# Performance work log

Measured on AMD Instinct MI355X. Metric: run time of the kernel, lower is better.

The kernel has to match this reference:

```python
import jax, jax.numpy as jnp
import numpy as np

B, C, N = 8, 128, 4096  # (batch, channels=dim, time); F = N//2+1 = 2049 (odd)


def setup_inputs() -> dict:
    key = jax.random.key(0)
    ks = jax.random.split(key, 7)
    s = 1.0 / np.sqrt(C)
    return {
        "x_in": jax.random.normal(ks[0], (B, C, N), dtype=jnp.float32),
        "W_K": jax.random.normal(ks[1], (C, C), dtype=jnp.float32) * s,
        "b_K": jax.random.normal(ks[2], (C,), dtype=jnp.float32) * s,
        "W_V": jax.random.normal(ks[3], (C, C), dtype=jnp.float32) * s,
        "b_V": jax.random.normal(ks[4], (C,), dtype=jnp.float32) * s,
        "w_high": jax.random.normal(ks[5], (C, 2), dtype=jnp.float32) * 0.02,
        "threshold_param": jax.random.uniform(ks[6], (1,), dtype=jnp.float32) * 0.5,
    }


def reference(x_in, W_K, b_K, W_V, b_V, w_high, threshold_param):
    x = jnp.transpose(x_in, (0, 2, 1)).astype(jnp.float32)  # (B, N, C)
    _, n, c = x.shape
    x_fft = jnp.fft.rfft(x, axis=1, norm="ortho")            # (B, F, C) complex64
    K = jnp.fft.rfft(x @ W_K.T + b_K, axis=1, norm="ortho")  # (B, F, C)
    V = jnp.fft.rfft(x @ W_V.T + b_V, axis=1, norm="ortho")  # (B, F, C)
    scale = c ** (-0.5)
    # complex attention scores (no conjugation, matching torch.matmul(Q, K^T))
    attn = jnp.einsum("bfc,bgc->bfg", x_fft, K) * scale      # (B, F, F) complex
    attn = jax.nn.softmax(jnp.abs(attn), axis=-1)            # real softmax of |scores|
    context = jnp.einsum("bfg,bgc->bfc", attn.astype(x_fft.dtype), V)
    # adaptive high-frequency mask
    energy = jnp.sum(jnp.abs(x_fft) ** 2, axis=-1)           # (B, F)
    median_energy = jnp.median(energy, axis=1, keepdims=True)
    normalized = energy / (median_energy + 1e-6)
    threshold = jnp.quantile(normalized, threshold_param[0])  # global quantile
    mask = (normalized > threshold)[:, :, None]               # (B, F, 1)
    w_hi = w_high[:, 0] + 1j * w_high[:, 1]                   # (C,) complex
    context = context + jnp.where(mask, x_fft, 0.0) * w_hi
    out = jnp.fft.irfft(context, n=n, axis=1, norm="ortho")  # (B, N, C) float32
    return jnp.transpose(out, (0, 2, 1))                      # (B, C, N)
```

## Files before the change

kernel.cpp:

```cpp
#include <hip/hip_runtime.h>
#include <math.h>

#define NB 8
#define NC 128
#define NT 4096
#define NF 2049
#define FP 2176
#define LDP 72

typedef __bf16 bf16;
typedef __bf16 bf16x2 __attribute__((ext_vector_type(2)));
typedef __bf16 bf16x8 __attribute__((ext_vector_type(8)));
typedef float f32x4 __attribute__((ext_vector_type(4)));
typedef unsigned int uint32x4 __attribute__((ext_vector_type(4)));

__device__ __forceinline__ void async16(const bf16* g, bf16* l) {
    __builtin_amdgcn_global_load_lds(
        (const __attribute__((address_space(1))) void*)g,
        (__attribute__((address_space(3))) void*)l, 16, 0, 0);
}

__device__ __forceinline__ bf16x8 derive_b2(bf16x8 v) {
    uint32x4 u = __builtin_bit_cast(uint32x4, v);
#pragma unroll
    for (int i = 0; i < 4; ++i)
        u[i] = (((u[i] >> 16) | (u[i] << 16)) ^ 0x00008000u);
    return __builtin_bit_cast(bf16x8, u);
}

__device__ __forceinline__ void fft4096(float2* buf) {
    for (int half = 1; half < NT; half <<= 1) {
        __syncthreads();
        const float fac = -(float)M_PI / (float)half;
        for (int t = threadIdx.x; t < NT / 2; t += 256) {
            int pos = t & (half - 1);
            int i = 2 * t - pos;
            int j = i + half;
            float sw, cw;
            __sincosf(fac * (float)pos, &sw, &cw);
            float2 u = buf[i], v = buf[j];
            float vr = v.x * cw - v.y * sw;
            float vi = v.x * sw + v.y * cw;
            buf[i] = make_float2(u.x + vr, u.y + vi);
            buf[j] = make_float2(u.x - vr, u.y - vi);
        }
    }
    __syncthreads();
}

__global__ __launch_bounds__(256) void fft_fwd_kernel(const float* __restrict__ x_in,
                                                      float2* __restrict__ Xc) {
    __shared__ float2 buf[NT];
    int bc = blockIdx.x;
    const float* xrow = x_in + (size_t)bc * NT;
    for (int i = threadIdx.x; i < NT; i += 256) {
        int r = __brev((unsigned)i) >> 20;
        buf[r] = make_float2(xrow[i], 0.0f);
    }
    fft4096(buf);
    const float inv = 1.0f / 64.0f;
    float2* orow = Xc + (size_t)bc * NF;
    for (int f = threadIdx.x; f < NF; f += 256) {
        float2 v = buf[f];
        orow[f] = make_float2(v.x * inv, v.y * inv);
    }
}

__global__ __launch_bounds__(256) void xt_kernel(const float2* __restrict__ Xc,
                                                 float2* __restrict__ Xf2,
                                                 bf16* __restrict__ Xb) {
    __shared__ float2 tile[64][65];
    int blk = blockIdx.x;
    int b = blk / 68;
    int t2 = blk % 68;
    int c0 = (t2 / 34) * 64;
    int f0 = (t2 % 34) * 64;
    int t = threadIdx.x;
    int fl = t & 63, cc = t >> 6;
#pragma unroll
    for (int cb = 0; cb < 16; ++cb) {
        int cl = cb * 4 + cc;
        int f = f0 + fl;
        float2 v = make_float2(0.f, 0.f);
        if (f < NF) v = Xc[((size_t)b * NC + c0 + cl) * NF + f];
        tile[fl][cl] = v;
    }
    __syncthreads();
    int chl = t & 63, ww = t >> 6;
#pragma unroll
    for (int wb = 0; wb < 16; ++wb) {
        int fl2 = wb * 4 + ww;
        int f = f0 + fl2;
        float2 v = tile[fl2][chl];
        if (f < NF) Xf2[((size_t)b * NF + f) * 128 + c0 + chl] = v;
        bf16x2 p;
        p[0] = (bf16)v.x; p[1] = (bf16)v.y;
        *(bf16x2*)&Xb[((size_t)b * FP + f) * 256 + 2 * (c0 + chl)] = p;
    }
}

__global__ __launch_bounds__(256) void wpack_kernel(const float* __restrict__ W_K,
                                                    const float* __restrict__ W_V,
                                                    bf16* __restrict__ Wk1,
                                                    bf16* __restrict__ Av) {
    int idx = blockIdx.x * 256 + threadIdx.x;
    if (idx < 256 * 256) {
        int n = idx >> 8, k = idx & 255;
        int c = k >> 1;
        int j = n >> 1;
        float v = 0.f;
        if (!(n & 1) && !(k & 1)) v = W_K[j * NC + c];
        else if ((n & 1) && (k & 1)) v = -W_K[j * NC + c];
        Wk1[idx] = (bf16)v;
        float v2 = 0.f;
        if (!(n & 1) && !(k & 1)) v2 = W_V[j * NC + c];
        else if ((n & 1) && (k & 1)) v2 = W_V[j * NC + c];
        Av[idx] = (bf16)v2;
    }
}

__global__ __launch_bounds__(256, 2) void kvgemm_kernel(const bf16* __restrict__ Xb,
                                                        const bf16* __restrict__ Wk1,
                                                        bf16* __restrict__ K1) {
    __shared__ bf16 As[128][LDP];
    __shared__ bf16 Bs[128][LDP];
    int blk = blockIdx.x;
    int b = blk & 7;
    int t2 = blk >> 3;
    int g0 = (t2 >> 1) * 128;
    int n0 = (t2 & 1) * 128;
    int tid = threadIdx.x;
    int wave = tid >> 6, lane = tid & 63;
    int m = lane & 15, quad = lane >> 4;
    int row_off = (wave & 1) * 64, col_off = (wave >> 1) * 64;

    f32x4 acc[4][4] = {};
    const bf16* Abase = Xb + ((size_t)b * FP + g0) * 256;
    const bf16* Bbase = Wk1 + (size_t)n0 * 256;
    int r0 = tid >> 3, c0 = (tid & 7) * 8;

    for (int kk = 0; kk < 256; kk += 64) {
        __syncthreads();
#pragma unroll
        for (int s = 0; s < 4; ++s) {
            int r = r0 + 32 * s;
            *(bf16x8*)&As[r][c0] = *(const bf16x8*)&Abase[(size_t)r * 256 + kk + c0];
            *(bf16x8*)&Bs[r][c0] = *(const bf16x8*)&Bbase[(size_t)r * 256 + kk + c0];
        }
        __syncthreads();
#pragma unroll
        for (int k2 = 0; k2 < 64; k2 += 32) {
            bf16x8 a[4], bb[4];
            int kq = k2 + quad * 8;
#pragma unroll
            for (int i = 0; i < 4; ++i) a[i] = *(const bf16x8*)&As[row_off + i * 16 + m][kq];
#pragma unroll
            for (int j = 0; j < 4; ++j) bb[j] = *(const bf16x8*)&Bs[col_off + j * 16 + m][kq];
#pragma unroll
            for (int i = 0; i < 4; ++i)
#pragma unroll
                for (int j = 0; j < 4; ++j)
                    acc[i][j] = __builtin_amdgcn_mfma_f32_16x16x32_bf16(a[i], bb[j], acc[i][j], 0, 0, 0);
        }
    }
#pragma unroll
    for (int i = 0; i < 4; ++i)
#pragma unroll
        for (int j = 0; j < 4; ++j)
#pragma unroll
            for (int r = 0; r < 4; ++r) {
                int row = g0 + row_off + i * 16 + quad * 4 + r;
                int col = n0 + col_off + j * 16 + m;
                K1[((size_t)b * FP + row) * 256 + col] = (bf16)acc[i][j][r];
            }
}

__global__ __launch_bounds__(256, 2) void vtgemm_kernel(const bf16* __restrict__ Av,
                                                        const bf16* __restrict__ Xb,
                                                        bf16* __restrict__ Vt) {
    __shared__ bf16 As[128][LDP];
    __shared__ bf16 Bs[128][LDP];
    int blk = blockIdx.x;
    int b = blk & 7;
    int t2 = blk >> 3;
    int g0 = (t2 >> 1) * 128;
    int n0 = (t2 & 1) * 128;
    int tid = threadIdx.x;
    int wave = tid >> 6, lane = tid & 63;
    int m = lane & 15, quad = lane >> 4;
    int row_off = (wave & 1) * 64, col_off = (wave >> 1) * 64;

    f32x4 acc[4][4] = {};
    const bf16* Abase = Av + (size_t)n0 * 256;
    const bf16* Bbase = Xb + ((size_t)b * FP + g0) * 256;
    int r0 = tid >> 3, c0 = (tid & 7) * 8;

    for (int kk = 0; kk < 256; kk += 64) {
        __syncthreads();
#pragma unroll
        for (int s = 0; s < 4; ++s) {
            int r = r0 + 32 * s;
            *(bf16x8*)&As[r][c0] = *(const bf16x8*)&Abase[(size_t)r * 256 + kk + c0];
            *(bf16x8*)&Bs[r][c0] = *(const bf16x8*)&Bbase[(size_t)r * 256 + kk + c0];
        }
        __syncthreads();
#pragma unroll
        for (int k2 = 0; k2 < 64; k2 += 32) {
            bf16x8 a[4], bb[4];
            int kq = k2 + quad * 8;
#pragma unroll
            for (int i = 0; i < 4; ++i) a[i] = *(const bf16x8*)&As[row_off + i * 16 + m][kq];
#pragma unroll
            for (int j = 0; j < 4; ++j) bb[j] = *(const bf16x8*)&Bs[col_off + j * 16 + m][kq];
#pragma unroll
            for (int i = 0; i < 4; ++i)
#pragma unroll
                for (int j = 0; j < 4; ++j)
                    acc[i][j] = __builtin_amdgcn_mfma_f32_16x16x32_bf16(a[i], bb[j], acc[i][j], 0, 0, 0);
        }
    }
#pragma unroll
    for (int i = 0; i < 4; ++i)
#pragma unroll
        for (int j = 0; j < 4; ++j)
#pragma unroll
            for (int r = 0; r < 4; ++r) {
                int row = n0 + row_off + i * 16 + quad * 4 + r;
                int col = g0 + col_off + j * 16 + m;
                Vt[((size_t)b * 256 + row) * FP + col] = (bf16)acc[i][j][r];
            }
}

__global__ __launch_bounds__(128) void biasfix_kernel(const float* __restrict__ b_K,
                                                      const float* __restrict__ b_V,
                                                      bf16* __restrict__ K1,
                                                      bf16* __restrict__ Vt) {
    int b = blockIdx.x;
    int j = threadIdx.x;
    float bk = 64.0f * b_K[j], bv = 64.0f * b_V[j];
    size_t o = (size_t)b * FP * 256;
    K1[o + 2 * j] = (bf16)((float)K1[o + 2 * j] + bk);
    size_t ov = ((size_t)b * 256 + 2 * j) * FP;
    Vt[ov] = (bf16)((float)Vt[ov] + bv);
}

__global__ __launch_bounds__(256) void energy_kernel(const float* __restrict__ Xf,
                                                     float* __restrict__ energy) {
    int idx = blockIdx.x * 256 + threadIdx.x;
    if (idx >= NB * NF) return;
    const float4* row = (const float4*)(Xf + (size_t)idx * 2 * NC);
    float e = 0.f;
    for (int i = 0; i < 64; ++i) {
        float4 v = row[i];
        e += v.x * v.x + v.y * v.y + v.z * v.z + v.w * v.w;
    }
    energy[idx] = e;
}

__global__ __launch_bounds__(256) void median_kernel(const float* __restrict__ energy,
                                                     float* __restrict__ med) {
    int blk = blockIdx.x;
    int b = blk / 9, chunk = blk % 9;
    __shared__ __align__(16) float e[2052];
    for (int i = threadIdx.x; i < 2052; i += 256)
        e[i] = (i < NF) ? energy[b * NF + i] : INFINITY;
    __syncthreads();
    int i = chunk * 256 + threadIdx.x;
    float ei = (i < NF) ? e[i] : 0.f;
    int rank = 0;
#pragma unroll 4
    for (int j4 = 0; j4 < 513; ++j4) {
        float4 v = ((const float4*)e)[j4];
        int j = j4 * 4;
        rank += (v.x < ei) || (v.x == ei && j + 0 < i);
        rank += (v.y < ei) || (v.y == ei && j + 1 < i);
        rank += (v.z < ei) || (v.z == ei && j + 2 < i);
        rank += (v.w < ei) || (v.w == ei && j + 3 < i);
    }
    if (i < NF && rank == 1024) med[b] = ei;
}

__global__ __launch_bounds__(256) void norm_kernel(const float* __restrict__ energy,
                                                   const float* __restrict__ med,
                                                   float* __restrict__ nrm) {
    int idx = blockIdx.x * 256 + threadIdx.x;
    if (idx >= NB * NF) return;
    int b = idx / NF;
    nrm[idx] = energy[idx] / (med[b] + 1e-6f);
}

__global__ __launch_bounds__(256) void rankpart_kernel(const float* __restrict__ nrm,
                                                       int* __restrict__ rankpart) {
    const int n = NB * NF;
    int cb = blockIdx.x / 17;
    int chunk = blockIdx.x % 17;
    __shared__ __align__(16) float cdata[1024];
    int base = chunk * 1024;
    for (int t = threadIdx.x; t < 1024; t += 256)
        cdata[t] = (base + t < n) ? nrm[base + t] : INFINITY;
    __syncthreads();
    int i = cb * 256 + threadIdx.x;
    if (i >= n) return;
    float ei = nrm[i];
    int rank = 0;
#pragma unroll 8
    for (int t4 = 0; t4 < 256; ++t4) {
        float4 v = ((const float4*)cdata)[t4];
        int j = base + t4 * 4;
        rank += (v.x < ei) || (v.x == ei && j + 0 < i);
        rank += (v.y < ei) || (v.y == ei && j + 1 < i);
        rank += (v.z < ei) || (v.z == ei && j + 2 < i);
        rank += (v.w < ei) || (v.w == ei && j + 3 < i);
    }
    rankpart[(size_t)i * 17 + chunk] = rank;
}

__global__ __launch_bounds__(256) void rankreduce_kernel(const int* __restrict__ rankpart,
                                                         const float* __restrict__ nrm,
                                                         const float* __restrict__ q,
                                                         float* __restrict__ vk) {
    const int n = NB * NF;
    int i = blockIdx.x * 256 + threadIdx.x;
    if (i >= n) return;
    int rank = 0;
    const int* rp = rankpart + (size_t)i * 17;
#pragma unroll
    for (int c = 0; c < 17; ++c) rank += rp[c];
    double pos = (double)q[0] * (double)(n - 1);
    int k0 = (int)floor(pos);
    int k1 = min(k0 + 1, n - 1);
    if (rank == k0) vk[0] = nrm[i];
    if (rank == k1) vk[1] = nrm[i];
}

__global__ void thresh_kernel(const float* __restrict__ vk,
                              const float* __restrict__ q,
                              float* __restrict__ thr) {
    if (threadIdx.x == 0 && blockIdx.x == 0) {
        const int n = NB * NF;
        double pos = (double)q[0] * (double)(n - 1);
        double k0 = floor(pos);
        double frac = pos - k0;
        thr[0] = (float)((double)vk[0] + ((double)vk[1] - (double)vk[0]) * frac);
    }
}

__global__ __launch_bounds__(256, 2) void score_kernel(const bf16* __restrict__ Xb,
                                                       const bf16* __restrict__ K1,
                                                       bf16* __restrict__ S) {
    __shared__ __align__(16) char smem[34816];
    bf16* As  = (bf16*)smem;
    bf16* B1s = (bf16*)(smem + 16384);
    int blk = blockIdx.x;
    int b = blk & 7;
    int t2 = blk >> 3;
    int f0 = (t2 / 17) * 128;
    int g0 = (t2 % 17) * 128;
    int tid = threadIdx.x;
    int wave = tid >> 6, lane = tid & 63;
    int m = lane & 15, quad = lane >> 4;
    int row_off = (wave & 1) * 64, col_off = (wave >> 1) * 64;

    f32x4 accRe[4][4] = {};
    f32x4 accIm[4][4] = {};
    const bf16* Abase = Xb + ((size_t)b * FP + f0) * 256;
    const bf16* Kbase = K1 + ((size_t)b * FP + g0) * 256;
    int lrow = lane >> 3;
    int cswz = (lane & 7) ^ lrow;
    int mk = m & 7;

    for (int kk = 0; kk < 256; kk += 64) {
        __syncthreads();
#pragma unroll
        for (int t = 0; t < 4; ++t) {
            int r0 = wave * 32 + t * 8;
            async16(Abase + (size_t)(r0 + lrow) * 256 + kk + cswz * 8, As + r0 * 64);
            async16(Kbase + (size_t)(r0 + lrow) * 256 + kk + cswz * 8, B1s + r0 * 64);
        }
        __syncthreads();
#pragma unroll
        for (int k2 = 0; k2 < 64; k2 += 32) {
            bf16x8 a[4], b1[4], b2[4];
            int cb = k2 >> 3;
            int pos = ((cb + quad) ^ mk) << 3;
#pragma unroll
            for (int i = 0; i < 4; ++i)
                a[i] = *(const bf16x8*)&As[(row_off + i * 16 + m) * 64 + pos];
#pragma unroll
            for (int j = 0; j < 4; ++j) {
                b1[j] = *(const bf16x8*)&B1s[(col_off + j * 16 + m) * 64 + pos];
                b2[j] = derive_b2(b1[j]);
            }
#pragma unroll
            for (int i = 0; i < 4; ++i)
#pragma unroll
                for (int j = 0; j < 4; ++j) {
                    accRe[i][j] = __builtin_amdgcn_mfma_f32_16x16x32_bf16(a[i], b1[j], accRe[i][j], 0, 0, 0);
                    accIm[i][j] = __builtin_amdgcn_mfma_f32_16x16x32_bf16(a[i], b2[j], accIm[i][j], 0, 0, 0);
                }
        }
    }
    const float SCALE = 0.08838834764831845f;
    __syncthreads();
    bf16 (*Cs)[136] = (bf16(*)[136])smem;
#pragma unroll
    for (int i = 0; i < 4; ++i)
#pragma unroll
        for (int j = 0; j < 4; ++j)
#pragma unroll
            for (int r = 0; r < 4; ++r) {
                float re = accRe[i][j][r], im = accIm[i][j][r];
                Cs[row_off + i * 16 + quad * 4 + r][col_off + j * 16 + m] =
                    (bf16)(sqrtf(re * re + im * im) * SCALE);
            }
    __syncthreads();
    bf16* Sb = S + (size_t)b * FP * FP;
    int row = tid >> 1, half = tid & 1;
    const bf16* src = &Cs[row][half * 64];
    bf16* dst = Sb + (size_t)(f0 + row) * FP + g0 + half * 64;
#pragma unroll
    for (int u = 0; u < 8; ++u)
        *(bf16x8*)&dst[u * 8] = *(const bf16x8*)&src[u * 8];
}

__global__ __launch_bounds__(256) void softmax_kernel(bf16* __restrict__ S) {
    int bf = blockIdx.x;
    int b = bf / NF, f = bf % NF;
    bf16* row = S + ((size_t)b * FP + f) * FP;
    int t = threadIdx.x;
    __shared__ float red[256];
    bf16x8 raw = *(const bf16x8*)&row[t * 8];
    float tail = (t == 0) ? (float)row[2048] : -1e30f;
    float v[8];
    float mx = tail;
#pragma unroll
    for (int u = 0; u < 8; ++u) { v[u] = (float)raw[u]; mx = fmaxf(mx, v[u]); }
    red[t] = mx;
    __syncthreads();
    for (int s = 128; s > 0; s >>= 1) {
        if (t < s) red[t] = fmaxf(red[t], red[t + s]);
        __syncthreads();
    }
    float mval = red[0];
    __syncthreads();
    float sum = 0.f;
#pragma unroll
    for (int u = 0; u < 8; ++u) { v[u] = __expf(v[u] - mval); sum += v[u]; }
    float tex = 0.f;
    if (t == 0) { tex = __expf(tail - mval); sum += tex; }
    red[t] = sum;
    __syncthreads();
    for (int s = 128; s > 0; s >>= 1) {
        if (t < s) red[t] += red[t + s];
        __syncthreads();
    }
    float inv = 1.f / red[0];
    bf16x8 outv;
#pragma unroll
    for (int u = 0; u < 8; ++u) outv[u] = (bf16)(v[u] * inv);
    *(bf16x8*)&row[t * 8] = outv;
    if (t == 0) row[2048] = (bf16)(tex * inv);
    if (t < FP - NF) row[NF + t] = (bf16)0.f;
}

__global__ __launch_bounds__(256, 2) void context_kernel(const bf16* __restrict__ P,
                                                         const bf16* __restrict__ Vt,
                                                         float* __restrict__ Ctx) {
    __shared__ bf16 Ps[64][LDP];
    __shared__ bf16 Vs[256][LDP];
    int blk = blockIdx.x;
    int b = blk & 7;
    int f0 = (blk >> 3) * 64;
    int tid = threadIdx.x;
    int wave = tid >> 6, lane = tid & 63;
    int m = lane & 15, quad = lane >> 4;
    int col_off = wave * 64;

    f32x4 acc[4][4] = {};
    const bf16* Pbase = P + ((size_t)b * FP + f0) * FP;
    const bf16* Vbase = Vt + (size_t)b * 256 * FP;
    int r0 = tid >> 3, c0 = (tid & 7) * 8;

    for (int kk = 0; kk < FP; kk += 64) {
        __syncthreads();
#pragma unroll
        for (int s = 0; s < 2; ++s) {
            int r = r0 + 32 * s;
            *(bf16x8*)&Ps[r][c0] = *(const bf16x8*)&Pbase[(size_t)r * FP + kk + c0];
        }
#pragma unroll
        for (int s = 0; s < 8; ++s) {
            int r = r0 + 32 * s;
            *(bf16x8*)&Vs[r][c0] = *(const bf16x8*)&Vbase[(size_t)r * FP + kk + c0];
        }
        __syncthreads();
#pragma unroll
        for (int k2 = 0; k2 < 64; k2 += 32) {
            bf16x8 a[4], bb[4];
            int kq = k2 + quad * 8;
#pragma unroll
            for (int i = 0; i < 4; ++i) a[i] = *(const bf16x8*)&Ps[i * 16 + m][kq];
#pragma unroll
            for (int j = 0; j < 4; ++j) bb[j] = *(const bf16x8*)&Vs[col_off + j * 16 + m][kq];
#pragma unroll
            for (int i = 0; i < 4; ++i)
#pragma unroll
                for (int j = 0; j < 4; ++j)
                    acc[i][j] = __builtin_amdgcn_mfma_f32_16x16x32_bf16(a[i], bb[j], acc[i][j], 0, 0, 0);
        }
    }
#pragma unroll
    for (int i = 0; i < 4; ++i)
#pragma unroll
        for (int j = 0; j < 4; ++j)
#pragma unroll
            for (int r = 0; r < 4; ++r) {
                int row = f0 + i * 16 + quad * 4 + r;
                int col = col_off + j * 16 + m;
                if (row < NF) Ctx[((size_t)b * NF + row) * 256 + col] = acc[i][j][r];
            }
}

__global__ __launch_bounds__(256) void ctxt_kernel(const float2* __restrict__ Ctx2,
                                                   const float2* __restrict__ Xf2,
                                                   const float* __restrict__ nrm,
                                                   const float* __restrict__ thr,
                                                   const float* __restrict__ w_high,
                                                   float* __restrict__ Ctxt) {
    __shared__ float2 tile[64][33];
    int blk = blockIdx.x;
    int b = blk / 132;
    int t2 = blk % 132;
    int cp0 = (t2 / 33) * 32;
    int f0 = (t2 % 33) * 64;
    int t = threadIdx.x;
    float thrv = thr[0];
    int cpl = t & 31, rr = t >> 5;
#pragma unroll
    for (int rb = 0; rb < 8; ++rb) {
        int fl = rb * 8 + rr;
        int f = f0 + fl;
        float2 v = make_float2(0.f, 0.f);
        if (f < NF) {
            size_t idx = ((size_t)b * NF + f) * 128 + cp0 + cpl;
            v = Ctx2[idx];
            if (nrm[b * NF + f] > thrv) {
                float2 x = Xf2[idx];
                int c = cp0 + cpl;
                float wr = w_high[2 * c], wi = w_high[2 * c + 1];
                v.x += x.x * wr - x.y * wi;
                v.y += x.x * wi + x.y * wr;
            }
        }
        tile[fl][cpl] = v;
    }
    __syncthreads();
    int fl = t & 63, ww = t >> 6;
#pragma unroll
    for (int wb = 0; wb < 16; ++wb) {
        int chl = wb * 4 + ww;
        int f = f0 + fl;
        if (f < NF) {
            float2 v = tile[fl][chl >> 1];
            Ctxt[((size_t)b * 256 + 2 * cp0 + chl) * NF + f] = (chl & 1) ? v.y : v.x;
        }
    }
}

__global__ __launch_bounds__(256) void fft_inv_kernel(const float* __restrict__ Ctxt,
                                                      float* __restrict__ out) {
    __shared__ float2 buf[NT];
    int bc = blockIdx.x, b = bc >> 7, c = bc & 127;
    const float* base = Ctxt + ((size_t)b * 256 + 2 * c) * NF;
    const float* basei = base + NF;
    for (int f = threadIdx.x; f < NT; f += 256) {
        float re, im;
        if (f <= NT / 2) {
            re = base[f];
            im = -basei[f];
        } else {
            int g = NT - f;
            re = base[g];
            im = basei[g];
        }
        int r = __brev((unsigned)f) >> 20;
        buf[r] = make_float2(re, im);
    }
    fft4096(buf);
    float* orow = out + (size_t)bc * NT;
    const float inv = 1.0f / 64.0f;
    for (int n = threadIdx.x; n < NT; n += 256) orow[n] = buf[n].x * inv;
}

extern "C" void kernel_launch(void* const* d_in, const int* in_sizes, int n_in,
                              void* d_out, int out_size, void* d_ws, size_t ws_size,
                              hipStream_t stream) {
    const float* x_in = (const float*)d_in[0];
    const float* W_K = (const float*)d_in[1];
    const float* b_K = (const float*)d_in[2];
    const float* W_V = (const float*)d_in[3];
    const float* b_V = (const float*)d_in[4];
    const float* w_high = (const float*)d_in[5];
    const float* qpar = (const float*)d_in[6];
    float* out = (float*)d_out;

    char* w = (char*)d_ws;
    const size_t SPECB = (size_t)NB * NF * 256 * 4;
    float* Xf = (float*)w;            w += SPECB;
    float* Ctx = (float*)w;           w += SPECB;
    float* energy = (float*)w;        w += (size_t)NB * NF * 4;
    float* med = (float*)w;           w += 64;
    float* nrm = (float*)w;           w += (size_t)NB * NF * 4;
    float* vk = (float*)w;            w += 64;
    float* thr = (float*)w;           w += 64;
    w = (char*)(((uintptr_t)w + 255) & ~(uintptr_t)255);
    int* rankpart = (int*)w;          w += (size_t)16640 * 17 * 4;
    w = (char*)(((uintptr_t)w + 255) & ~(uintptr_t)255);
    bf16* S = (bf16*)w;               w += (size_t)NB * FP * FP * 2;
    bf16* Xb = (bf16*)w;              w += (size_t)NB * FP * 256 * 2;
    bf16* K1 = (bf16*)w;              w += (size_t)NB * FP * 256 * 2;
    bf16* Vt = (bf16*)w;              w += (size_t)NB * 256 * FP * 2;
    bf16* Wk1 = (bf16*)w;             w += (size_t)256 * 256 * 2;
    bf16* Av = (bf16*)w;              w += (size_t)256 * 256 * 2;
    float2* Xc = (float2*)S;
    float* Ctxt = (float*)Xb;

    fft_fwd_kernel<<<NB * NC, 256, 0, stream>>>(x_in, Xc);
    xt_kernel<<<NB * 2 * 34, 256, 0, stream>>>(Xc, (float2*)Xf, Xb);
    wpack_kernel<<<256, 256, 0, stream>>>(W_K, W_V, Wk1, Av);
    kvgemm_kernel<<<NB * 17 * 2, 256, 0, stream>>>(Xb, Wk1, K1);
    vtgemm_kernel<<<NB * 17 * 2, 256, 0, stream>>>(Av, Xb, Vt);
    biasfix_kernel<<<NB, 128, 0, stream>>>(b_K, b_V, K1, Vt);
    energy_kernel<<<(NB * NF + 255) / 256, 256, 0, stream>>>(Xf, energy);
    median_kernel<<<NB * 9, 256, 0, stream>>>(energy, med);
    norm_kernel<<<(NB * NF + 255) / 256, 256, 0, stream>>>(energy, med, nrm);
    rankpart_kernel<<<65 * 17, 256, 0, stream>>>(nrm, rankpart);
    rankreduce_kernel<<<65, 256, 0, stream>>>(rankpart, nrm, qpar, vk);
    thresh_kernel<<<1, 64, 0, stream>>>(vk, qpar, thr);
    score_kernel<<<NB * 17 * 17, 256, 0, stream>>>(Xb, K1, S);
    softmax_kernel<<<NB * NF, 256, 0, stream>>>(S);
    context_kernel<<<NB * 33, 256, 0, stream>>>(S, Vt, Ctx);
    ctxt_kernel<<<NB * 4 * 33, 256, 0, stream>>>((const float2*)Ctx, (const float2*)Xf,
                                                 nrm, thr, w_high, Ctxt);
    fft_inv_kernel<<<NB * NC, 256, 0, stream>>>(Ctxt, out);
}
```

Before: 433.8 us.

## Fuse score, softmax and context GEMMs into a single flash-attention kernel

Replaces the separate score GEMM, row softmax and context GEMM kernels with one kernel that uses an online softmax. Each block keeps 64 query rows resident and streams K and V tiles through shared memory, computing |score| tiles, running max/sum and PV accumulation in registers. This removes the large bf16 score matrix and its write/read/rewrite passes through global memory, and the score workspace is dropped, with the FFT scratch now aliased into Ctx. The trade-off is that all the score compute is serialised into only 264 blocks, with several barriers per tile and no double-buffering, so latency may be exposed.

```diff
diff --git a/kernel.cpp b/kernel.cpp
--- a/kernel.cpp
+++ b/kernel.cpp
@@ -345,180 +345,174 @@
     }
 }
 
-__global__ __launch_bounds__(256, 2) void score_kernel(const bf16* __restrict__ Xb,
+__global__ __launch_bounds__(256, 2) void flash_kernel(const bf16* __restrict__ Xb,
                                                        const bf16* __restrict__ K1,
-                                                       bf16* __restrict__ S) {
-    __shared__ __align__(16) char smem[34816];
-    bf16* As  = (bf16*)smem;
-    bf16* B1s = (bf16*)(smem + 16384);
-    int blk = blockIdx.x;
-    int b = blk & 7;
-    int t2 = blk >> 3;
-    int f0 = (t2 / 17) * 128;
-    int g0 = (t2 % 17) * 128;
-    int tid = threadIdx.x;
-    int wave = tid >> 6, lane = tid & 63;
-    int m = lane & 15, quad = lane >> 4;
-    int row_off = (wave & 1) * 64, col_off = (wave >> 1) * 64;
-
-    f32x4 accRe[4][4] = {};
-    f32x4 accIm[4][4] = {};
-    const bf16* Abase = Xb + ((size_t)b * FP + f0) * 256;
-    const bf16* Kbase = K1 + ((size_t)b * FP + g0) * 256;
-    int lrow = lane >> 3;
-    int cswz = (lane & 7) ^ lrow;
-    int mk = m & 7;
-
-    for (int kk = 0; kk < 256; kk += 64) {
-        __syncthreads();
-#pragma unroll
-        for (int t = 0; t < 4; ++t) {
-            int r0 = wave * 32 + t * 8;
-            async16(Abase + (size_t)(r0 + lrow) * 256 + kk + cswz * 8, As + r0 * 64);
-            async16(Kbase + (size_t)(r0 + lrow) * 256 + kk + cswz * 8, B1s + r0 * 64);
-        }
-        __syncthreads();
-#pragma unroll
-        for (int k2 = 0; k2 < 64; k2 += 32) {
-            bf16x8 a[4], b1[4], b2[4];
-            int cb = k2 >> 3;
-            int pos = ((cb + quad) ^ mk) << 3;
-#pragma unroll
-            for (int i = 0; i < 4; ++i)
-                a[i] = *(const bf16x8*)&As[(row_off + i * 16 + m) * 64 + pos];
-#pragma unroll
-            for (int j = 0; j < 4; ++j) {
-                b1[j] = *(const bf16x8*)&B1s[(col_off + j * 16 + m) * 64 + pos];
-                b2[j] = derive_b2(b1[j]);
-            }
-#pragma unroll
-            for (int i = 0; i < 4; ++i)
-#pragma unroll
-                for (int j = 0; j < 4; ++j) {
-                    accRe[i][j] = __builtin_amdgcn_mfma_f32_16x16x32_bf16(a[i], b1[j], accRe[i][j], 0, 0, 0);
-                    accIm[i][j] = __builtin_amdgcn_mfma_f32_16x16x32_bf16(a[i], b2[j], accIm[i][j], 0, 0, 0);
-                }
-        }
-    }
-    const float SCALE = 0.08838834764831845f;
-    __syncthreads();
-    bf16 (*Cs)[136] = (bf16(*)[136])smem;
-#pragma unroll
-    for (int i = 0; i < 4; ++i)
-#pragma unroll
-        for (int j = 0; j < 4; ++j)
-#pragma unroll
-            for (int r = 0; r < 4; ++r) {
-                float re = accRe[i][j][r], im = accIm[i][j][r];
-                Cs[row_off + i * 16 + quad * 4 + r][col_off + j * 16 + m] =
-                    (bf16)(sqrtf(re * re + im * im) * SCALE);
-            }
-    __syncthreads();
-    bf16* Sb = S + (size_t)b * FP * FP;
-    int row = tid >> 1, half = tid & 1;
-    const bf16* src = &Cs[row][half * 64];
-    bf16* dst = Sb + (size_t)(f0 + row) * FP + g0 + half * 64;
-#pragma unroll
-    for (int u = 0; u < 8; ++u)
-        *(bf16x8*)&dst[u * 8] = *(const bf16x8*)&src[u * 8];
-}
-
-__global__ __launch_bounds__(256) void softmax_kernel(bf16* __restrict__ S) {
-    int bf = blockIdx.x;
-    int b = bf / NF, f = bf % NF;
-    bf16* row = S + ((size_t)b * FP + f) * FP;
-    int t = threadIdx.x;
-    __shared__ float red[256];
-    bf16x8 raw = *(const bf16x8*)&row[t * 8];
-    float tail = (t == 0) ? (float)row[2048] : -1e30f;
-    float v[8];
-    float mx = tail;
-#pragma unroll
-    for (int u = 0; u < 8; ++u) { v[u] = (float)raw[u]; mx = fmaxf(mx, v[u]); }
-    red[t] = mx;
-    __syncthreads();
-    for (int s = 128; s > 0; s >>= 1) {
-        if (t < s) red[t] = fmaxf(red[t], red[t + s]);
-        __syncthreads();
-    }
-    float mval = red[0];
-    __syncthreads();
-    float sum = 0.f;
-#pragma unroll
-    for (int u = 0; u < 8; ++u) { v[u] = __expf(v[u] - mval); sum += v[u]; }
-    float tex = 0.f;
-    if (t == 0) { tex = __expf(tail - mval); sum += tex; }
-    red[t] = sum;
-    __syncthreads();
-    for (int s = 128; s > 0; s >>= 1) {
-        if (t < s) red[t] += red[t + s];
-        __syncthreads();
-    }
-    float inv = 1.f / red[0];
-    bf16x8 outv;
-#pragma unroll
-    for (int u = 0; u < 8; ++u) outv[u] = (bf16)(v[u] * inv);
-    *(bf16x8*)&row[t * 8] = outv;
-    if (t == 0) row[2048] = (bf16)(tex * inv);
-    if (t < FP - NF) row[NF + t] = (bf16)0.f;
-}
-
-__global__ __launch_bounds__(256, 2) void context_kernel(const bf16* __restrict__ P,
-                                                         const bf16* __restrict__ Vt,
-                                                         float* __restrict__ Ctx) {
-    __shared__ bf16 Ps[64][LDP];
-    __shared__ bf16 Vs[256][LDP];
+                                                       const bf16* __restrict__ Vt,
+                                                       float* __restrict__ Ctx) {
+    __shared__ __align__(16) char smem[65536];
+    bf16* As = (bf16*)smem;
+    bf16* KV = (bf16*)(smem + 32768);
+    bf16* Pw = (bf16*)(smem + 32768 + 16384);
     int blk = blockIdx.x;
     int b = blk & 7;
     int f0 = (blk >> 3) * 64;
     int tid = threadIdx.x;
     int wave = tid >> 6, lane = tid & 63;
     int m = lane & 15, quad = lane >> 4;
-    int col_off = wave * 64;
-
-    f32x4 acc[4][4] = {};
-    const bf16* Pbase = P + ((size_t)b * FP + f0) * FP;
-    const bf16* Vbase = Vt + (size_t)b * 256 * FP;
-    int r0 = tid >> 3, c0 = (tid & 7) * 8;
-
-    for (int kk = 0; kk < FP; kk += 64) {
-        __syncthreads();
-#pragma unroll
-        for (int s = 0; s < 2; ++s) {
-            int r = r0 + 32 * s;
-            *(bf16x8*)&Ps[r][c0] = *(const bf16x8*)&Pbase[(size_t)r * FP + kk + c0];
-        }
-#pragma unroll
-        for (int s = 0; s < 8; ++s) {
-            int r = r0 + 32 * s;
-            *(bf16x8*)&Vs[r][c0] = *(const bf16x8*)&Vbase[(size_t)r * FP + kk + c0];
-        }
-        __syncthreads();
-#pragma unroll
-        for (int k2 = 0; k2 < 64; k2 += 32) {
-            bf16x8 a[4], bb[4];
-            int kq = k2 + quad * 8;
-#pragma unroll
-            for (int i = 0; i < 4; ++i) a[i] = *(const bf16x8*)&Ps[i * 16 + m][kq];
-#pragma unroll
-            for (int j = 0; j < 4; ++j) bb[j] = *(const bf16x8*)&Vs[col_off + j * 16 + m][kq];
-#pragma unroll
-            for (int i = 0; i < 4; ++i)
-#pragma unroll
-                for (int j = 0; j < 4; ++j)
-                    acc[i][j] = __builtin_amdgcn_mfma_f32_16x16x32_bf16(a[i], bb[j], acc[i][j], 0, 0, 0);
-        }
-    }
-#pragma unroll
-    for (int i = 0; i < 4; ++i)
-#pragma unroll
-        for (int j = 0; j < 4; ++j)
+    int lrow = lane >> 3;
+    int cswz = (lane & 7) ^ lrow;
+    int mk = m & 7;
+    const float SCALE = 0.08838834764831845f;
+
+    const bf16* Ab = Xb + ((size_t)b * FP + f0) * 256;
+    const bf16* Kb = K1 + (size_t)b * FP * 256;
+    const bf16* Vb = Vt + (size_t)b * 256 * FP;
+
+#pragma unroll
+    for (int p = 0; p < 4; ++p)
+#pragma unroll
+        for (int t = 0; t < 2; ++t) {
+            int r0 = wave * 16 + t * 8;
+            async16(Ab + (size_t)(r0 + lrow) * 256 + p * 64 + cswz * 8,
+                    As + p * 4096 + r0 * 64);
+        }
+
+    float mrow[4] = {-1e30f, -1e30f, -1e30f, -1e30f};
+    float lsum[4] = {0.f, 0.f, 0.f, 0.f};
+    f32x4 o[16] = {};
+
+    for (int gi = 0; gi < 33; ++gi) {
+        int g0 = gi * 64;
+        __syncthreads();
+#pragma unroll
+        for (int p = 0; p < 4; ++p)
+#pragma unroll
+            for (int t = 0; t < 2; ++t) {
+                int r0 = wave * 16 + t * 8;
+                async16(Kb + (size_t)(g0 + r0 + lrow) * 256 + p * 64 + cswz * 8,
+                        KV + p * 4096 + r0 * 64);
+            }
+        __syncthreads();
+
+        f32x4 accRe[4] = {};
+        f32x4 accIm[4] = {};
+#pragma unroll
+        for (int ks = 0; ks < 8; ++ks) {
+            int p = ks >> 1;
+            int pos = (((ks & 1) * 4 + quad) ^ mk) << 3;
+            bf16x8 a = *(const bf16x8*)&As[p * 4096 + (wave * 16 + m) * 64 + pos];
+#pragma unroll
+            for (int j2 = 0; j2 < 4; ++j2) {
+                bf16x8 b1 = *(const bf16x8*)&KV[p * 4096 + (j2 * 16 + m) * 64 + pos];
+                bf16x8 b2 = derive_b2(b1);
+                accRe[j2] = __builtin_amdgcn_mfma_f32_16x16x32_bf16(a, b1, accRe[j2], 0, 0, 0);
+                accIm[j2] = __builtin_amdgcn_mfma_f32_16x16x32_bf16(a, b2, accIm[j2], 0, 0, 0);
+            }
+        }
+
+        float pv[4][4];
+        float tmax[4] = {-1e30f, -1e30f, -1e30f, -1e30f};
+#pragma unroll
+        for (int j2 = 0; j2 < 4; ++j2) {
+            int gcol = g0 + j2 * 16 + m;
+            bool valid = (gcol <= 2048);
 #pragma unroll
             for (int r = 0; r < 4; ++r) {
-                int row = f0 + i * 16 + quad * 4 + r;
-                int col = col_off + j * 16 + m;
-                if (row < NF) Ctx[((size_t)b * NF + row) * 256 + col] = acc[i][j][r];
-            }
+                float re = accRe[j2][r], im = accIm[j2][r];
+                float s = valid ? sqrtf(re * re + im * im) * SCALE : -1e30f;
+                pv[j2][r] = s;
+                tmax[r] = fmaxf(tmax[r], s);
+            }
+        }
+#pragma unroll
+        for (int r = 0; r < 4; ++r) {
+            tmax[r] = fmaxf(tmax[r], __shfl_xor(tmax[r], 1));
+            tmax[r] = fmaxf(tmax[r], __shfl_xor(tmax[r], 2));
+            tmax[r] = fmaxf(tmax[r], __shfl_xor(tmax[r], 4));
+            tmax[r] = fmaxf(tmax[r], __shfl_xor(tmax[r], 8));
+        }
+        float alpha[4], rs[4];
+#pragma unroll
+        for (int r = 0; r < 4; ++r) {
+            float mn = fmaxf(mrow[r], tmax[r]);
+            alpha[r] = __expf(mrow[r] - mn);
+            mrow[r] = mn;
+            rs[r] = 0.f;
+        }
+#pragma unroll
+        for (int j2 = 0; j2 < 4; ++j2)
+#pragma unroll
+            for (int r = 0; r < 4; ++r) {
+                float e = __expf(pv[j2][r] - mrow[r]);
+                pv[j2][r] = e;
+                rs[r] += e;
+            }
+#pragma unroll
+        for (int r = 0; r < 4; ++r) {
+            rs[r] += __shfl_xor(rs[r], 1);
+            rs[r] += __shfl_xor(rs[r], 2);
+            rs[r] += __shfl_xor(rs[r], 4);
+            rs[r] += __shfl_xor(rs[r], 8);
+            lsum[r] = lsum[r] * alpha[r] + rs[r];
+        }
+#pragma unroll
+        for (int j = 0; j < 16; ++j)
+#pragma unroll
+            for (int r = 0; r < 4; ++r) o[j][r] *= alpha[r];
+
+        __syncthreads();
+#pragma unroll
+        for (int t = 0; t < 4; ++t) {
+            int n0 = wave * 32 + t * 8;
+            async16(Vb + (size_t)(n0 + lrow) * FP + g0 + cswz * 8, KV + n0 * 64);
+        }
+#pragma unroll
+        for (int j2 = 0; j2 < 4; ++j2)
+#pragma unroll
+            for (int r = 0; r < 4; ++r)
+                Pw[(wave * 16 + quad * 4 + r) * 72 + j2 * 16 + m] = (bf16)pv[j2][r];
+        __syncthreads();
+
+        bf16x8 pa[2];
+#pragma unroll
+        for (int ks2 = 0; ks2 < 2; ++ks2) {
+            pa[ks2] = *(const bf16x8*)&Pw[(wave * 16 + m) * 72 + ks2 * 32 + quad * 8];
+            int pos = ((ks2 * 4 + quad) ^ mk) << 3;
+#pragma unroll
+            for (int j = 0; j < 8; ++j) {
+                bf16x8 vb = *(const bf16x8*)&KV[(j * 16 + m) * 64 + pos];
+                o[j] = __builtin_amdgcn_mfma_f32_16x16x32_bf16(pa[ks2], vb, o[j], 0, 0, 0);
+            }
+        }
+        __syncthreads();
+#pragma unroll
+        for (int t = 0; t < 4; ++t) {
+            int n0 = 128 + wave * 32 + t * 8;
+            async16(Vb + (size_t)(n0 + lrow) * FP + g0 + cswz * 8, KV + (n0 - 128) * 64);
+        }
+        __syncthreads();
+#pragma unroll
+        for (int ks2 = 0; ks2 < 2; ++ks2) {
+            int pos = ((ks2 * 4 + quad) ^ mk) << 3;
+#pragma unroll
+            for (int j = 8; j < 16; ++j) {
+                bf16x8 vb = *(const bf16x8*)&KV[((j - 8) * 16 + m) * 64 + pos];
+                o[j] = __builtin_amdgcn_mfma_f32_16x16x32_bf16(pa[ks2], vb, o[j], 0, 0, 0);
+            }
+        }
+    }
+
+    float inv[4];
+#pragma unroll
+    for (int r = 0; r < 4; ++r) inv[r] = 1.f / lsum[r];
+#pragma unroll
+    for (int j = 0; j < 16; ++j)
+#pragma unroll
+        for (int r = 0; r < 4; ++r) {
+            int row = f0 + wave * 16 + quad * 4 + r;
+            if (row < NF)
+                Ctx[((size_t)b * NF + row) * 256 + j * 16 + m] = o[j][r] * inv[r];
+        }
 }
 
 __global__ __launch_bounds__(256) void ctxt_kernel(const float2* __restrict__ Ctx2,
@@ -616,13 +610,12 @@
     w = (char*)(((uintptr_t)w + 255) & ~(uintptr_t)255);
     int* rankpart = (int*)w;          w += (size_t)16640 * 17 * 4;
     w = (char*)(((uintptr_t)w + 255) & ~(uintptr_t)255);
-    bf16* S = (bf16*)w;               w += (size_t)NB * FP * FP * 2;
     bf16* Xb = (bf16*)w;              w += (size_t)NB * FP * 256 * 2;
     bf16* K1 = (bf16*)w;              w += (size_t)NB * FP * 256 * 2;
     bf16* Vt = (bf16*)w;              w += (size_t)NB * 256 * FP * 2;
     bf16* Wk1 = (bf16*)w;             w += (size_t)256 * 256 * 2;
     bf16* Av = (bf16*)w;              w += (size_t)256 * 256 * 2;
-    float2* Xc = (float2*)S;
+    float2* Xc = (float2*)Ctx;
     float* Ctxt = (float*)Xb;
 
     fft_fwd_kernel<<<NB * NC, 256, 0, stream>>>(x_in, Xc);
@@ -637,9 +630,7 @@
     rankpart_kernel<<<65 * 17, 256, 0, stream>>>(nrm, rankpart);
     rankreduce_kernel<<<65, 256, 0, stream>>>(rankpart, nrm, qpar, vk);
     thresh_kernel<<<1, 64, 0, stream>>>(vk, qpar, thr);
-    score_kernel<<<NB * 17 * 17, 256, 0, stream>>>(Xb, K1, S);
-    softmax_kernel<<<NB * NF, 256, 0, stream>>>(S);
-    context_kernel<<<NB * 33, 256, 0, stream>>>(S, Vt, Ctx);
+    flash_kernel<<<NB * 33, 256, 0, stream>>>(Xb, K1, Vt, Ctx);
     ctxt_kernel<<<NB * 4 * 33, 256, 0, stream>>>((const float2*)Ctx, (const float2*)Xf,
                                                  nrm, thr, w_high, Ctxt);
     fft_inv_kernel<<<NB * NC, 256, 0, stream>>>(Ctxt, out);
```

Result: slower. 489.2 us (+12.8%).

## Use direct global-to-LDS async loads with XOR-swizzled layout in GEMM kernels

Applied to the files above, without the earlier changes.

Replaces the register-staged global-to-shared copies in the K, V and context GEMM kernels with global_load_lds 16-byte async transfers. The padded LDS rows (stride 72) become unpadded 64-wide rows with an XOR column swizzle, to avoid bank conflicts without padding and to skip the VGPR round trip. The context kernel's launch bound drops its minimum-blocks hint. The loads are still synchronised with barriers rather than double-buffered, so transfer latency is not overlapped with compute.

```diff
diff --git a/kernel.cpp b/kernel.cpp
--- a/kernel.cpp
+++ b/kernel.cpp
@@ -6,7 +6,6 @@
 #define NT 4096
 #define NF 2049
 #define FP 2176
-#define LDP 72
 
 typedef __bf16 bf16;
 typedef __bf16 bf16x2 __attribute__((ext_vector_type(2)));
@@ -122,8 +121,8 @@
 __global__ __launch_bounds__(256, 2) void kvgemm_kernel(const bf16* __restrict__ Xb,
                                                         const bf16* __restrict__ Wk1,
                                                         bf16* __restrict__ K1) {
-    __shared__ bf16 As[128][LDP];
-    __shared__ bf16 Bs[128][LDP];
+    __shared__ __align__(16) bf16 As[128 * 64];
+    __shared__ __align__(16) bf16 Bs[128 * 64];
     int blk = blockIdx.x;
     int b = blk & 7;
     int t2 = blk >> 3;
@@ -133,29 +132,31 @@
     int wave = tid >> 6, lane = tid & 63;
     int m = lane & 15, quad = lane >> 4;
     int row_off = (wave & 1) * 64, col_off = (wave >> 1) * 64;
+    int lrow = lane >> 3;
+    int cswz = (lane & 7) ^ lrow;
+    int mk = m & 7;
 
     f32x4 acc[4][4] = {};
     const bf16* Abase = Xb + ((size_t)b * FP + g0) * 256;
     const bf16* Bbase = Wk1 + (size_t)n0 * 256;
-    int r0 = tid >> 3, c0 = (tid & 7) * 8;
 
     for (int kk = 0; kk < 256; kk += 64) {
         __syncthreads();
 #pragma unroll
-        for (int s = 0; s < 4; ++s) {
-            int r = r0 + 32 * s;
-            *(bf16x8*)&As[r][c0] = *(const bf16x8*)&Abase[(size_t)r * 256 + kk + c0];
-            *(bf16x8*)&Bs[r][c0] = *(const bf16x8*)&Bbase[(size_t)r * 256 + kk + c0];
+        for (int t = 0; t < 4; ++t) {
+            int r0 = wave * 32 + t * 8;
+            async16(Abase + (size_t)(r0 + lrow) * 256 + kk + cswz * 8, As + r0 * 64);
+            async16(Bbase + (size_t)(r0 + lrow) * 256 + kk + cswz * 8, Bs + r0 * 64);
         }
         __syncthreads();
 #pragma unroll
         for (int k2 = 0; k2 < 64; k2 += 32) {
             bf16x8 a[4], bb[4];
-            int kq = k2 + quad * 8;
-#pragma unroll
-            for (int i = 0; i < 4; ++i) a[i] = *(const bf16x8*)&As[row_off + i * 16 + m][kq];
-#pragma unroll
-            for (int j = 0; j < 4; ++j) bb[j] = *(const bf16x8*)&Bs[col_off + j * 16 + m][kq];
+            int pos = (((k2 >> 3) + quad) ^ mk) << 3;
+#pragma unroll
+            for (int i = 0; i < 4; ++i) a[i] = *(const bf16x8*)&As[(row_off + i * 16 + m) * 64 + pos];
+#pragma unroll
+            for (int j = 0; j < 4; ++j) bb[j] = *(const bf16x8*)&Bs[(col_off + j * 16 + m) * 64 + pos];
 #pragma unroll
             for (int i = 0; i < 4; ++i)
 #pragma unroll
@@ -178,8 +179,8 @@
 __global__ __launch_bounds__(256, 2) void vtgemm_kernel(const bf16* __restrict__ Av,
                                                         const bf16* __restrict__ Xb,
                                                         bf16* __restrict__ Vt) {
-    __shared__ bf16 As[128][LDP];
-    __shared__ bf16 Bs[128][LDP];
+    __shared__ __align__(16) bf16 As[128 * 64];
+    __shared__ __align__(16) bf16 Bs[128 * 64];
     int blk = blockIdx.x;
     int b = blk & 7;
     int t2 = blk >> 3;
@@ -189,29 +190,31 @@
     int wave = tid >> 6, lane = tid & 63;
     int m = lane & 15, quad = lane >> 4;
     int row_off = (wave & 1) * 64, col_off = (wave >> 1) * 64;
+    int lrow = lane >> 3;
+    int cswz = (lane & 7) ^ lrow;
+    int mk = m & 7;
 
     f32x4 acc[4][4] = {};
     const bf16* Abase = Av + (size_t)n0 * 256;
     const bf16* Bbase = Xb + ((size_t)b * FP + g0) * 256;
-    int r0 = tid >> 3, c0 = (tid & 7) * 8;
 
     for (int kk = 0; kk < 256; kk += 64) {
         __syncthreads();
 #pragma unroll
-        for (int s = 0; s < 4; ++s) {
-            int r = r0 + 32 * s;
-            *(bf16x8*)&As[r][c0] = *(const bf16x8*)&Abase[(size_t)r * 256 + kk + c0];
-            *(bf16x8*)&Bs[r][c0] = *(const bf16x8*)&Bbase[(size_t)r * 256 + kk + c0];
+        for (int t = 0; t < 4; ++t) {
+            int r0 = wave * 32 + t * 8;
+            async16(Abase + (size_t)(r0 + lrow) * 256 + kk + cswz * 8, As + r0 * 64);
+            async16(Bbase + (size_t)(r0 + lrow) * 256 + kk + cswz * 8, Bs + r0 * 64);
         }
         __syncthreads();
 #pragma unroll
         for (int k2 = 0; k2 < 64; k2 += 32) {
             bf16x8 a[4], bb[4];
-            int kq = k2 + quad * 8;
-#pragma unroll
-            for (int i = 0; i < 4; ++i) a[i] = *(const bf16x8*)&As[row_off + i * 16 + m][kq];
-#pragma unroll
-            for (int j = 0; j < 4; ++j) bb[j] = *(const bf16x8*)&Bs[col_off + j * 16 + m][kq];
+            int pos = (((k2 >> 3) + quad) ^ mk) << 3;
+#pragma unroll
+            for (int i = 0; i < 4; ++i) a[i] = *(const bf16x8*)&As[(row_off + i * 16 + m) * 64 + pos];
+#pragma unroll
+            for (int j = 0; j < 4; ++j) bb[j] = *(const bf16x8*)&Bs[(col_off + j * 16 + m) * 64 + pos];
 #pragma unroll
             for (int i = 0; i < 4; ++i)
 #pragma unroll
@@ -463,11 +466,11 @@
     if (t < FP - NF) row[NF + t] = (bf16)0.f;
 }
 
-__global__ __launch_bounds__(256, 2) void context_kernel(const bf16* __restrict__ P,
-                                                         const bf16* __restrict__ Vt,
-                                                         float* __restrict__ Ctx) {
-    __shared__ bf16 Ps[64][LDP];
-    __shared__ bf16 Vs[256][LDP];
+__global__ __launch_bounds__(256) void context_kernel(const bf16* __restrict__ P,
+                                                      const bf16* __restrict__ Vt,
+                                                      float* __restrict__ Ctx) {
+    __shared__ __align__(16) bf16 Ps[64 * 64];
+    __shared__ __align__(16) bf16 Vs[256 * 64];
     int blk = blockIdx.x;
     int b = blk & 7;
     int f0 = (blk >> 3) * 64;
@@ -475,33 +478,35 @@
     int wave = tid >> 6, lane = tid & 63;
     int m = lane & 15, quad = lane >> 4;
     int col_off = wave * 64;
+    int lrow = lane >> 3;
+    int cswz = (lane & 7) ^ lrow;
+    int mk = m & 7;
 
     f32x4 acc[4][4] = {};
     const bf16* Pbase = P + ((size_t)b * FP + f0) * FP;
     const bf16* Vbase = Vt + (size_t)b * 256 * FP;
-    int r0 = tid >> 3, c0 = (tid & 7) * 8;
 
     for (int kk = 0; kk < FP; kk += 64) {
         __syncthreads();
 #pragma unroll
-        for (int s = 0; s < 2; ++s) {
-            int r = r0 + 32 * s;
-            *(bf16x8*)&Ps[r][c0] = *(const bf16x8*)&Pbase[(size_t)r * FP + kk + c0];
-        }
-#pragma unroll
-        for (int s = 0; s < 8; ++s) {
-            int r = r0 + 32 * s;
-            *(bf16x8*)&Vs[r][c0] = *(const bf16x8*)&Vbase[(size_t)r * FP + kk + c0];
+        for (int t = 0; t < 2; ++t) {
+            int r0 = wave * 16 + t * 8;
+            async16(Pbase + (size_t)(r0 + lrow) * FP + kk + cswz * 8, Ps + r0 * 64);
+        }
+#pragma unroll
+        for (int t = 0; t < 8; ++t) {
+            int r0 = wave * 64 + t * 8;
+            async16(Vbase + (size_t)(r0 + lrow) * FP + kk + cswz * 8, Vs + r0 * 64);
         }
         __syncthreads();
 #pragma unroll
         for (int k2 = 0; k2 < 64; k2 += 32) {
             bf16x8 a[4], bb[4];
-            int kq = k2 + quad * 8;
-#pragma unroll
-            for (int i = 0; i < 4; ++i) a[i] = *(const bf16x8*)&Ps[i * 16 + m][kq];
-#pragma unroll
-            for (int j = 0; j < 4; ++j) bb[j] = *(const bf16x8*)&Vs[col_off + j * 16 + m][kq];
+            int pos = (((k2 >> 3) + quad) ^ mk) << 3;
+#pragma unroll
+            for (int i = 0; i < 4; ++i) a[i] = *(const bf16x8*)&Ps[(i * 16 + m) * 64 + pos];
+#pragma unroll
+            for (int j = 0; j < 4; ++j) bb[j] = *(const bf16x8*)&Vs[(col_off + j * 16 + m) * 64 + pos];
 #pragma unroll
             for (int i = 0; i < 4; ++i)
 #pragma unroll
```

After: 435.9 us. No clear change (+0.5%).
